# Performance work log

Measured on AMD Instinct MI355X. Metric: run time of the kernel, lower is better.

## Reference

```python
import jax, jax.numpy as jnp
import numpy as np

N, C, H, W = 4, 256, 64, 64
S = 2          # scale_factor
K = 5          # up_kernel
G = 1          # up_group
CK = 64        # compressed_channels


def conv2d(x, w, b, pad):
    out = jax.lax.conv_general_dilated(
        x, w, window_strides=(1, 1), padding=[(pad, pad), (pad, pad)],
        dimension_numbers=('NCHW', 'OIHW', 'NCHW'))
    return out + b[None, :, None, None]


def pixel_shuffle(x, r):
    n, cr, h, w = x.shape
    c = cr // (r * r)
    return x.reshape(n, c, r, r, h, w).transpose(0, 1, 4, 2, 5, 3).reshape(n, c, h * r, w * r)


def grid_sample_border(img, grid):
    # img [N,C,Hi,Wi], grid [N,Ho,Wo,2] in [-1,1] (x,y); bilinear, border pad, align_corners=True
    n, c, hi, wi = img.shape
    gx = (grid[..., 0] + 1.0) * 0.5 * (wi - 1)
    gy = (grid[..., 1] + 1.0) * 0.5 * (hi - 1)
    gx = jnp.clip(gx, 0.0, wi - 1.0)
    gy = jnp.clip(gy, 0.0, hi - 1.0)
    x0 = jnp.floor(gx).astype(jnp.int32)
    y0 = jnp.floor(gy).astype(jnp.int32)
    x1 = jnp.minimum(x0 + 1, wi - 1)
    y1 = jnp.minimum(y0 + 1, hi - 1)
    wx = (gx - x0)[..., None]
    wy = (gy - y0)[..., None]
    bidx = jnp.arange(n)[:, None, None]
    def gather(yy, xx):
        return img[bidx, :, yy, xx]  # [N,Ho,Wo,C]
    v00 = gather(y0, x0)
    v01 = gather(y0, x1)
    v10 = gather(y1, x0)
    v11 = gather(y1, x1)
    out = (v00 * (1 - wx) * (1 - wy) + v01 * wx * (1 - wy)
           + v10 * (1 - wx) * wy + v11 * wx * wy)
    return out.transpose(0, 3, 1, 2)


def carafe2(features, masks, k, g, up):
    n, c, h, w = features.shape
    cg = c // g
    k2 = k * k
    # masks [N, g*k2, h*up, w*up] -> per-pixel kernels [n,g,h,w,k2,up2]
    m = masks.reshape(n, g, k2, h, up, w, up)
    m = m.transpose(0, 1, 2, 3, 5, 4, 6).reshape(n, g, k2, h, w, up * up)
    kern = m.transpose(0, 1, 3, 4, 2, 5)            # [n,g,h,w,k2,up2]
    f = features.reshape(n, g, cg, h, w)
    p = k // 2
    fp = jnp.pad(f, ((0, 0), (0, 0), (0, 0), (p, p), (p, p)))
    patches = jnp.stack([fp[:, :, :, i:i + h, j:j + w]
                         for i in range(k) for j in range(k)], axis=-1)  # [n,g,cg,h,w,k2]
    xp = patches.transpose(0, 1, 3, 4, 2, 5)        # [n,g,h,w,cg,k2]
    out = jnp.einsum('nghwck,nghwku->nghwcu', xp, kern)  # [n,g,h,w,cg,up2]
    out = out.transpose(0, 1, 4, 2, 3, 5).reshape(n, c * up * up, h, w)
    return pixel_shuffle(out, up)


def setup_inputs() -> dict:
    key = jax.random.key(0)
    ks = jax.random.split(key, 4)
    x = jax.random.normal(ks[0], (N, C, H, W), dtype=jnp.float32)
    w_comp = jax.random.normal(ks[1], (CK, C, 1, 1), dtype=jnp.float32) * 0.05
    b_comp = jnp.zeros((CK,), dtype=jnp.float32)
    w_ker = jax.random.normal(ks[2], (G * K * K, CK, 3, 3), dtype=jnp.float32) * 0.001
    b_ker = jnp.zeros((G * K * K,), dtype=jnp.float32)
    w_off = jax.random.normal(ks[3], (G * 2 * S * S, CK, 3, 3), dtype=jnp.float32) * 0.01
    b_off = jnp.zeros((G * 2 * S * S,), dtype=jnp.float32)
    return {'x': x, 'w_comp': w_comp, 'b_comp': b_comp,
            'w_ker': w_ker, 'b_ker': b_ker, 'w_off': w_off, 'b_off': b_off}


def reference(x, w_comp, b_comp, w_ker, b_ker, w_off, b_off):
    cx = conv2d(x, w_comp, b_comp, 0)               # channel compressor (1x1)
    offset = conv2d(cx, w_off, b_off, 1)            # [N, 2*S*S, H, W]
    mask = conv2d(cx, w_ker, b_ker, 1)              # [N, G*K*K, H, W]
    # kernel_space_normalizer: softmax over the K*K kernel positions
    n, mc, h, w = mask.shape
    mask = jax.nn.softmax(mask.reshape(n, mc // (K * K), K * K, h, w), axis=2)
    mask = mask.reshape(n, mc, h, w)
    # kernel_space_expander
    off = pixel_shuffle(offset, S).transpose(0, 2, 3, 1)  # [N, H*S, W*S, 2]
    off = off * jnp.array([2.0 / (w - 1), 2.0 / (h - 1)], dtype=off.dtype)
    gh = jnp.repeat(jnp.linspace(-1.0, 1.0, h), S)  # [H*S]
    gw = jnp.repeat(jnp.linspace(-1.0, 1.0, w), S)  # [W*S]
    base = jnp.stack(jnp.broadcast_arrays(gw[None, :], gh[:, None]), axis=-1)  # [H*S, W*S, 2]
    grid = base[None] + off
    mask_ = grid_sample_border(mask, grid)          # [N, G*K*K, H*S, W*S]
    return carafe2(x, mask_, K, G, S)
```

## Files before the change

kernel.cpp:

```cpp
#include <hip/hip_runtime.h>
#include <math.h>

#define NB 4
#define C_IN 256
#define CKC 64
#define HWSZ 4096
#define K2 25
#define NOC2 40

#define WS_CX    0
#define WS_OFF   (WS_CX + NB*CKC*HWSZ)
#define WS_MASK  (WS_OFF + NB*8*HWSZ)
#define WS_WT    (WS_MASK + NB*K2*HWSZ)

#define NWT (CKC * 9 * NOC2)
#define NWC (C_IN * CKC)

__global__ void k_wt(const float* __restrict__ wk, const float* __restrict__ wo,
                     const float* __restrict__ wc,
                     float* __restrict__ wT, float* __restrict__ wcT) {
  int i = blockIdx.x * 256 + threadIdx.x;
  if (i < NWT) {
    int oc = i % NOC2;
    int r = i / NOC2;
    int tap = r % 9, c = r / 9;
    float v = 0.f;
    if (oc < 8)       v = wo[(oc * CKC + c) * 9 + tap];
    else if (oc < 33) v = wk[((oc - 8) * CKC + c) * 9 + tap];
    wT[i] = v;
  } else {
    int j = i - NWT;
    if (j < NWC) {
      int c = j >> 6, ck = j & 63;
      wcT[j] = wc[ck * C_IN + c];
    }
  }
}

__global__ __launch_bounds__(512) void k_compress(const float* __restrict__ x,
    const float* __restrict__ wcT, const float* __restrict__ bc,
    float* __restrict__ cx) {
  __shared__ float s_x[64 * 64];
  int t = threadIdx.x;
  int pos0 = blockIdx.x * 64;
  int n = pos0 >> 12, hw0 = pos0 & 4095;
  int p = t & 63;
  int g = __builtin_amdgcn_readfirstlane(t >> 6);
  const float* xn = x + (size_t)n * (C_IN * HWSZ) + hw0;
  float acc[8];
  #pragma unroll
  for (int i = 0; i < 8; i++) acc[i] = bc[g * 8 + i];
  for (int cc = 0; cc < 4; cc++) {
    __syncthreads();
    #pragma unroll
    for (int it = 0; it < 8; it++) {
      int idx = t + it * 512;
      int c = idx >> 6, pp = idx & 63;
      s_x[idx] = xn[(cc * 64 + c) * HWSZ + pp];
    }
    __syncthreads();
    const float* wbase = wcT + (cc * 64) * 64 + g * 8;
    #pragma unroll 4
    for (int c = 0; c < 64; c++) {
      float v = s_x[c * 64 + p];
      const float* w = wbase + c * 64;
      #pragma unroll
      for (int i = 0; i < 8; i++) acc[i] += v * w[i];
    }
  }
  float* o = cx + (size_t)n * (CKC * HWSZ) + hw0 + p;
  #pragma unroll
  for (int i = 0; i < 8; i++) o[(g * 8 + i) * HWSZ] = acc[i];
}

__global__ __launch_bounds__(512) void k_convsm(const float* __restrict__ cx,
    const float* __restrict__ wT, const float* __restrict__ bk, const float* __restrict__ bo,
    float* __restrict__ offb, float* __restrict__ maskb) {
  __shared__ float s_tile[64 * 108];
  __shared__ float s_res[NOC2 * 64];
  int t = threadIdx.x;
  int n = blockIdx.y;
  int tile = blockIdx.x;
  int x0 = (tile & 3) * 16, y0 = (tile >> 2) * 4;
  const float* cxn = cx + n * (CKC * HWSZ);

  for (int idx = t; idx < 6912; idx += 512) {
    int c = idx / 108;
    int rem = idx - c * 108;
    int row = rem / 18, col = rem - row * 18;
    int gy = y0 - 1 + row, gx = x0 - 1 + col;
    float v = 0.f;
    if ((unsigned)gy < 64u && (unsigned)gx < 64u) v = cxn[c * HWSZ + gy * 64 + gx];
    s_tile[idx] = v;
  }
  __syncthreads();

  int p = t & 63;
  int px = p & 15, py = p >> 4;
  int g = __builtin_amdgcn_readfirstlane(t >> 6);
  float acc[5];
  #pragma unroll
  for (int j = 0; j < 5; j++) acc[j] = 0.f;
  const float* wg = wT + g * 5;
  for (int c = 0; c < CKC; c++) {
    const float* tl = s_tile + c * 108 + py * 18 + px;
    const float* wc9 = wg + c * 9 * NOC2;
    #pragma unroll
    for (int tap = 0; tap < 9; tap++) {
      int dy = tap / 3, dx = tap % 3;
      float v = tl[dy * 18 + dx];
      const float* w = wc9 + tap * NOC2;
      #pragma unroll
      for (int j = 0; j < 5; j++) acc[j] += v * w[j];
    }
  }
  #pragma unroll
  for (int j = 0; j < 5; j++) s_res[(g * 5 + j) * 64 + p] = acc[j];
  __syncthreads();

  int hw = (y0 + py) * 64 + x0 + px;
  offb[(n * 8 + g) * HWSZ + hw] = s_res[g * 64 + p] + bo[g];
  if (t < 64) {
    float m[25], mx = -1e30f;
    #pragma unroll
    for (int k = 0; k < 25; k++) { m[k] = s_res[(8 + k) * 64 + p] + bk[k]; mx = fmaxf(mx, m[k]); }
    float s = 0.f;
    #pragma unroll
    for (int k = 0; k < 25; k++) { m[k] = __expf(m[k] - mx); s += m[k]; }
    float inv = 1.f / s;
    #pragma unroll
    for (int k = 0; k < 25; k++) maskb[(n * 25 + k) * HWSZ + hw] = m[k] * inv;
  }
}

__global__ __launch_bounds__(256, 4) void k_carafe(const float* __restrict__ x,
    const float* __restrict__ offb, const float* __restrict__ maskb,
    float* __restrict__ out) {
  __attribute__((aligned(16))) __shared__ float s_patch[32 * 201];
  __attribute__((aligned(16))) __shared__ float s_kern[32 * 25 * 4];
  int t = threadIdx.x;
  int b = blockIdx.x;
  int n = b >> 8;
  int r = b & 255;
  int half = r & 1;
  int wq = (r >> 1) & 3;
  int aa = r >> 3;
  int a = aa + (aa & 16);
  int yout = (a & 15) * 8 + wq * 2 + ((a >> 5) & 1);
  int w0 = wq * 16;
  int cbase = n * C_IN + half * 128;

  if (t < 128) {
    int p = t >> 2, u = t & 3;
    int hb = p >> 4, wl = p & 15;
    int h = a + hb * 16;
    int wcol = w0 + wl;
    float ox = offb[(n * 8 + u) * HWSZ + h * 64 + wcol];
    float oy = offb[(n * 8 + 4 + u) * HWSZ + h * 64 + wcol];
    float gx = fminf(fmaxf((float)wcol + ox, 0.f), 63.f);
    float gy = fminf(fmaxf((float)h + oy, 0.f), 63.f);
    float fx0 = floorf(gx), fy0 = floorf(gy);
    int x0 = (int)fx0, y0 = (int)fy0;
    float fx = gx - fx0, fy = gy - fy0;
    int x1 = min(x0 + 1, 63), y1 = min(y0 + 1, 63);
    float w11 = fx * fy;
    float w10 = fy - w11, w01 = fx - w11, w00 = 1.f - fx - fy + w11;
    const float* mb = maskb + n * (K2 * HWSZ);
    int i00 = y0 * 64 + x0, i01 = y0 * 64 + x1;
    int i10 = y1 * 64 + x0, i11 = y1 * 64 + x1;
    #pragma unroll 5
    for (int k = 0; k < 25; k++) {
      const float* mk = mb + k * HWSZ;
      float v = w00 * mk[i00] + w01 * mk[i01] + w10 * mk[i10] + w11 * mk[i11];
      s_kern[(p * 25 + k) * 4 + u] = v;
    }
  }

  int cl = t & 31, g = t >> 5;
  int hb = g >> 2, wl0 = (g & 3) * 4;
  float* s_out = s_patch;

  for (int cc = 0; cc < 4; cc++) {
    __syncthreads();
    const float* xn = x + (size_t)(cbase + cc * 32) * HWSZ;
    for (int idx = t; idx < 6400; idx += 256) {
      int c = idx / 200;
      int rem = idx - c * 200;
      int rg = rem / 20;
      int col = rem - rg * 20;
      int row = (rg < 5) ? (a - 2 + rg) : (a + 9 + rg);
      int gc = w0 - 2 + col;
      float v = 0.f;
      if ((unsigned)row < 64u && (unsigned)gc < 64u)
        v = xn[c * HWSZ + row * 64 + gc];
      s_patch[c * 201 + rem] = v;
    }
    __syncthreads();
    float acc[4][4];
    #pragma unroll
    for (int i = 0; i < 4; i++)
      acc[i][0] = acc[i][1] = acc[i][2] = acc[i][3] = 0.f;
    const float* pc = s_patch + cl * 201 + hb * 100 + wl0;
    #pragma unroll
    for (int dy = 0; dy < 5; dy++) {
      float r8[8];
      #pragma unroll
      for (int j = 0; j < 8; j++) r8[j] = pc[dy * 20 + j];
      #pragma unroll
      for (int pr = 0; pr < 4; pr++) {
        const float4* kp = (const float4*)(s_kern + (((g * 4 + pr) * 25) + dy * 5) * 4);
        #pragma unroll
        for (int dx = 0; dx < 5; dx++) {
          float f = r8[pr + dx];
          float4 k4 = kp[dx];
          acc[pr][0] += f * k4.x;
          acc[pr][1] += f * k4.y;
          acc[pr][2] += f * k4.z;
          acc[pr][3] += f * k4.w;
        }
      }
    }
    __syncthreads();
    #pragma unroll
    for (int pr = 0; pr < 4; pr++) {
      int wl = wl0 + pr;
      #pragma unroll
      for (int u = 0; u < 4; u++) {
        int xo = wl * 8 + u * 2 + hb;
        s_out[cl * 130 + xo] = acc[pr][u];
      }
    }
    __syncthreads();
    float* obase = out + ((size_t)(cbase + cc * 32) * 128 + yout) * 128;
    #pragma unroll
    for (int it = 0; it < 4; it++) {
      int q = t + it * 256;
      int rowc = q >> 5;
      int col4 = q & 31;
      const float* sp = s_out + rowc * 130 + col4 * 4;
      float4 v = make_float4(sp[0], sp[1], sp[2], sp[3]);
      *(float4*)(obase + (size_t)rowc * (128 * 128) + col4 * 4) = v;
    }
  }
}

extern "C" void kernel_launch(void* const* d_in, const int* in_sizes, int n_in,
                              void* d_out, int out_size, void* d_ws, size_t ws_size,
                              hipStream_t stream) {
  const float* x      = (const float*)d_in[0];
  const float* w_comp = (const float*)d_in[1];
  const float* b_comp = (const float*)d_in[2];
  const float* w_ker  = (const float*)d_in[3];
  const float* b_ker  = (const float*)d_in[4];
  const float* w_off  = (const float*)d_in[5];
  const float* b_off  = (const float*)d_in[6];
  float* out = (float*)d_out;
  float* ws = (float*)d_ws;
  float* cx    = ws + WS_CX;
  float* offb  = ws + WS_OFF;
  float* maskb = ws + WS_MASK;
  float* wT    = ws + WS_WT;
  float* wcT   = ws + WS_MASK;

  hipLaunchKernelGGL(k_wt, dim3((NWT + NWC + 255) / 256), dim3(256), 0, stream,
                     w_ker, w_off, w_comp, wT, wcT);
  hipLaunchKernelGGL(k_compress, dim3(256), dim3(512), 0, stream, x, wcT, b_comp, cx);
  hipLaunchKernelGGL(k_convsm, dim3(64, 4), dim3(512), 0, stream,
                     cx, wT, b_ker, b_off, offb, maskb);
  hipLaunchKernelGGL(k_carafe, dim3(1024), dim3(256), 0, stream, x, offb, maskb, out);
}
```

Measured before the change: 205.8 us.

## Prefetch next channel chunk into registers and precompute gather offsets

The per-thread gather offsets, validity bits and channel indices for the 25 patch-load iterations are computed once before the channel loop instead of being recomputed for every chunk. Global loads for the next 32-channel chunk are issued into registers right after the shared-memory store, so their latency overlaps the current chunk's FMA work. This adds about 50 live registers per thread (offsets plus prefetched values), which could lower occupancy under the 256x4 launch bounds or cause spills.

```diff
diff --git a/kernel.cpp b/kernel.cpp
--- a/kernel.cpp
+++ b/kernel.cpp
@@ -149,6 +149,31 @@
   int yout = (a & 15) * 8 + wq * 2 + ((a >> 5) & 1);
   int w0 = wq * 16;
   int cbase = n * C_IN + half * 128;
+
+  int srcOff[25];
+  unsigned cpack[5] = {0, 0, 0, 0, 0};
+  unsigned vbits = 0;
+  #pragma unroll
+  for (int it = 0; it < 25; it++) {
+    int idx = t + it * 256;
+    int c = idx / 200;
+    int rem = idx - c * 200;
+    int rg = rem / 20;
+    int col = rem - rg * 20;
+    int row = (rg < 5) ? (a - 2 + rg) : (a + 9 + rg);
+    int gc = w0 - 2 + col;
+    bool ok = ((unsigned)row < 64u) & ((unsigned)gc < 64u);
+    srcOff[it] = ok ? (c * HWSZ + row * 64 + gc) : 0;
+    vbits |= (ok ? 1u : 0u) << it;
+    cpack[it / 6] |= (unsigned)c << ((it % 6) * 5);
+  }
+
+  float rv[25];
+  {
+    const float* xn = x + (size_t)cbase * HWSZ;
+    #pragma unroll
+    for (int it = 0; it < 25; it++) rv[it] = xn[srcOff[it]];
+  }
 
   if (t < 128) {
     int p = t >> 2, u = t & 3;
@@ -182,20 +207,18 @@
 
   for (int cc = 0; cc < 4; cc++) {
     __syncthreads();
-    const float* xn = x + (size_t)(cbase + cc * 32) * HWSZ;
-    for (int idx = t; idx < 6400; idx += 256) {
-      int c = idx / 200;
-      int rem = idx - c * 200;
-      int rg = rem / 20;
-      int col = rem - rg * 20;
-      int row = (rg < 5) ? (a - 2 + rg) : (a + 9 + rg);
-      int gc = w0 - 2 + col;
-      float v = 0.f;
-      if ((unsigned)row < 64u && (unsigned)gc < 64u)
-        v = xn[c * HWSZ + row * 64 + gc];
-      s_patch[c * 201 + rem] = v;
-    }
-    __syncthreads();
+    #pragma unroll
+    for (int it = 0; it < 25; it++) {
+      int c = (cpack[it / 6] >> ((it % 6) * 5)) & 31;
+      float v = (vbits & (1u << it)) ? rv[it] : 0.f;
+      s_patch[t + it * 256 + c] = v;
+    }
+    __syncthreads();
+    if (cc < 3) {
+      const float* xn = x + (size_t)(cbase + (cc + 1) * 32) * HWSZ;
+      #pragma unroll
+      for (int it = 0; it < 25; it++) rv[it] = xn[srcOff[it]];
+    }
     float acc[4][4];
     #pragma unroll
     for (int i = 0; i < 4; i++)
```

New measurement: 198.2 us. -3.7%, faster.
